# Performance work log

Measured on AMD Instinct MI355X. Metric: run time of the kernel, lower is better.

The kernel has to match this reference:

```python
import jax, jax.numpy as jnp
import numpy as np

EMB = 1024
H = 16
D = EMB // H  # 64
EPS = 1e-5
SM_SCALE = 1.0  # forward default sm_scale=1.0
CAUSAL = True
NEG = -1e30


def _layernorm(t, g, b):
    # LayerNorm over last dim (head_dim), per torch nn.LayerNorm(head_dim)
    m = jnp.mean(t, axis=-1, keepdims=True)
    v = jnp.mean(jnp.square(t - m), axis=-1, keepdims=True)
    return (t - m) * jax.lax.rsqrt(v + EPS) * g + b


def setup_inputs() -> dict:
    key = jax.random.key(0)
    ks = jax.random.split(key, 8)
    N, L = 2, 2048
    x = jax.random.normal(ks[0], (N, L, EMB), dtype=jnp.float32)
    mask = jnp.ones((N, L), dtype=jnp.int32)  # accepted but unused, as in the torch module
    s = 0.02
    Wq = jax.random.normal(ks[1], (EMB, EMB), dtype=jnp.float32) * s
    Wk = jax.random.normal(ks[2], (EMB, EMB), dtype=jnp.float32) * s
    Wv = jax.random.normal(ks[3], (EMB, EMB), dtype=jnp.float32) * s
    Wo = jax.random.normal(ks[4], (EMB, EMB), dtype=jnp.float32) * s
    bo = jnp.zeros((EMB,), dtype=jnp.float32)
    gq = jnp.ones((D,), dtype=jnp.float32)
    bq = jnp.zeros((D,), dtype=jnp.float32)
    gk = jnp.ones((D,), dtype=jnp.float32)
    bk = jnp.zeros((D,), dtype=jnp.float32)
    return {"x": x, "mask": mask, "Wq": Wq, "Wk": Wk, "Wv": Wv,
            "gq": gq, "bq": bq, "gk": gk, "bk": bk, "Wo": Wo, "bo": bo}


def reference(x, mask, Wq, Wk, Wv, gq, bq, gk, bk, Wo, bo):
    N, L, _ = x.shape
    # QKV projections (torch Linear: x @ W.T), split into heads -> [N, H, L, D]
    q = (x @ Wq.T).reshape(N, L, H, D).transpose(0, 2, 1, 3)
    k = (x @ Wk.T).reshape(N, L, H, D).transpose(0, 2, 1, 3)
    v = (x @ Wv.T).reshape(N, L, H, D).transpose(0, 2, 1, 3)
    # fused_q_norm variant: per-head LayerNorm on Q and K (fused into attention kernel)
    q = _layernorm(q, gq, bq)
    k = _layernorm(k, gk, bk)
    scores = jnp.einsum('nhld,nhmd->nhlm', q, k) * SM_SCALE  # [N,H,L,L]
    if CAUSAL:
        causal = jnp.tril(jnp.ones((L, L), dtype=bool))
        scores = jnp.where(causal, scores, NEG)
    attn = jax.nn.softmax(scores, axis=-1)
    out = jnp.einsum('nhlm,nhmd->nhld', attn, v)
    out = out.transpose(0, 2, 1, 3).reshape(N, L, EMB)
    return out @ Wo.T + bo
```

## Files before the change

kernel.cpp:

```cpp
#include <hip/hip_runtime.h>
#include <stdint.h>

typedef unsigned short u16;
typedef u16   u16x4    __attribute__((ext_vector_type(4)));
typedef u16   u16x8    __attribute__((ext_vector_type(8)));
typedef u16x8 u16x8_ma __attribute__((may_alias));
typedef __bf16 bf16x8  __attribute__((ext_vector_type(8)));
typedef float f32x4    __attribute__((ext_vector_type(4)));
typedef f32x4 f32x4_ma __attribute__((may_alias));

#define EMB    1024
#define NHEAD  16
#define HD     64
#define SEQ    2048
#define NBATCH 2
#define ROWS   (NBATCH*SEQ)
#define SATT   72

__device__ __forceinline__ u16 f2b(float f) {
  uint32_t u; __builtin_memcpy(&u, &f, 4);
  u = u + 0x7fffu + ((u >> 16) & 1u);
  return (u16)(u >> 16);
}
__device__ __forceinline__ u16x8 ld8(const u16* p) { return *(const u16x8_ma*)p; }
__device__ __forceinline__ void  st8(u16* p, u16x8 v) { *(u16x8_ma*)p = v; }
__device__ __forceinline__ bf16x8 asbf(u16x8 v) {
  union { u16x8 u; bf16x8 b; } c; c.u = v; return c.b;
}
__device__ __forceinline__ uint32_t cvtpk(float a, float b) {
  uint32_t r;
  asm("v_cvt_pk_bf16_f32 %0, %1, %2" : "=v"(r) : "v"(a), "v"(b));
  return r;
}
__device__ __forceinline__ void async_cp16(const u16* g, u16* l) {
  __builtin_amdgcn_global_load_lds(
      (const __attribute__((address_space(1))) void*)g,
      (__attribute__((address_space(3))) void*)l, 16, 0, 0);
}

__global__ __launch_bounds__(256) void cvt_all(
    const float* __restrict__ x,
    const float* __restrict__ w0, const float* __restrict__ w1,
    const float* __restrict__ w2, const float* __restrict__ w3,
    u16* __restrict__ xd, u16* __restrict__ d0, u16* __restrict__ d1,
    u16* __restrict__ d2, u16* __restrict__ d3)
{
  int bid = blockIdx.x;
  const float* s; u16* d; int off;
  if (bid < 4096) { s = x; d = xd; off = bid; }
  else {
    int t = bid - 4096; int m = t >> 10; off = t & 1023;
    switch (m) {
      case 0: s = w0; d = d0; break;
      case 1: s = w1; d = d1; break;
      case 2: s = w2; d = d2; break;
      default: s = w3; d = d3; break;
    }
  }
  size_t i = ((size_t)off * 256 + threadIdx.x) * 4;
  f32x4 v = *(const f32x4_ma*)(s + i);
  u16x4 o;
  #pragma unroll
  for (int j = 0; j < 4; j++) o[j] = f2b(v[j]);
  *(u16x4*)(d + i) = o;
}

template<int AMODE>
__device__ __forceinline__ void gemm_acc_128x128(
    const u16* __restrict__ A, const u16* __restrict__ B,
    int m0, int n0, u16* As, u16* Bs, f32x4 acc[4][4])
{
  const int tid  = threadIdx.x;
  const int lane = tid & 63;
  const int wave = tid >> 6;
  const int wm   = (wave >> 1) * 64;
  const int wn   = (wave & 1) * 64;
  const int ar   = tid >> 2;
  const int ac   = (tid & 3) * 8;
  const int lm   = lane & 15;
  const int lk   = (lane >> 4) * 8;

  #pragma unroll
  for (int i = 0; i < 4; i++)
    #pragma unroll
    for (int j = 0; j < 4; j++)
      #pragma unroll
      for (int e = 0; e < 4; e++) acc[i][j][e] = 0.f;

  for (int k0 = 0; k0 < EMB; k0 += 64) {
    size_t a0[2], a1[2];
    #pragma unroll
    for (int pnl = 0; pnl < 2; pnl++) {
      int kc = k0 + pnl * 32 + ac;
      if (AMODE == 0) {
        a0[pnl] = (size_t)(m0 + ar)      * EMB + kc;
        a1[pnl] = (size_t)(m0 + ar + 64) * EMB + kc;
      } else {
        int h = kc >> 6, d = kc & 63;
        int r0 = m0 + ar, r1 = m0 + ar + 64;
        a0[pnl] = (((size_t)((r0 >> 11) * NHEAD + h)) * SEQ + (r0 & (SEQ-1))) * HD + d;
        a1[pnl] = (((size_t)((r1 >> 11) * NHEAD + h)) * SEQ + (r1 & (SEQ-1))) * HD + d;
      }
    }
    __syncthreads();
    #pragma unroll
    for (int pnl = 0; pnl < 2; pnl++) {
      const int pb = pnl * 4096;
      async_cp16(A + a0[pnl], As + pb + tid * 8);
      async_cp16(A + a1[pnl], As + pb + (tid + 256) * 8);
      async_cp16(B + (size_t)(n0 + ar)      * EMB + k0 + pnl * 32 + ac, Bs + pb + tid * 8);
      async_cp16(B + (size_t)(n0 + ar + 64) * EMB + k0 + pnl * 32 + ac, Bs + pb + (tid + 256) * 8);
    }
    __syncthreads();

    #pragma unroll
    for (int pnl = 0; pnl < 2; pnl++) {
      const int pb = pnl * 4096;
      bf16x8 af[4], bfr[4];
      #pragma unroll
      for (int i = 0; i < 4; i++)
        af[i] = asbf(ld8(As + pb + (wm + i * 16 + lm) * 32 + lk));
      #pragma unroll
      for (int j = 0; j < 4; j++)
        bfr[j] = asbf(ld8(Bs + pb + (wn + j * 16 + lm) * 32 + lk));
      #pragma unroll
      for (int i = 0; i < 4; i++)
        #pragma unroll
        for (int j = 0; j < 4; j++)
          acc[i][j] = __builtin_amdgcn_mfma_f32_16x16x32_bf16(af[i], bfr[j], acc[i][j], 0, 0, 0);
    }
  }
}

__device__ __forceinline__ void epilogue_scatter_ln(
    f32x4 acc[4][4], u16* dst, int m0, int n0, int head_base, int Hdst,
    const float* g, const float* b, int do_ln)
{
  const int lane = threadIdx.x & 63, wave = threadIdx.x >> 6;
  const int wm = (wave >> 1) * 64, wn = (wave & 1) * 64;
  const int lm = lane & 15, quad = lane >> 4;

  float gv[4], bv[4];
  #pragma unroll
  for (int j = 0; j < 4; j++) { gv[j] = g[j * 16 + lm]; bv[j] = b[j * 16 + lm]; }

  #pragma unroll
  for (int i = 0; i < 4; i++)
    #pragma unroll
    for (int r = 0; r < 4; r++) {
      float val[4];
      #pragma unroll
      for (int j = 0; j < 4; j++) val[j] = acc[i][j][r];
      if (do_ln) {
        float s = val[0] + val[1] + val[2] + val[3];
        #pragma unroll
        for (int o = 8; o >= 1; o >>= 1) s += __shfl_xor(s, o, 64);
        float mean = s * (1.f / 64.f);
        float ss = 0.f;
        #pragma unroll
        for (int j = 0; j < 4; j++) { val[j] -= mean; ss += val[j] * val[j]; }
        #pragma unroll
        for (int o = 8; o >= 1; o >>= 1) ss += __shfl_xor(ss, o, 64);
        float inv = rsqrtf(ss * (1.f / 64.f) + 1e-5f);
        #pragma unroll
        for (int j = 0; j < 4; j++) val[j] = val[j] * inv * gv[j] + bv[j];
      }
      int row = m0 + wm + i * 16 + quad * 4 + r;
      int bn = row >> 11, l = row & (SEQ - 1);
      #pragma unroll
      for (int j = 0; j < 4; j++) {
        int col = n0 + wn + j * 16 + lm;
        int hl = (col >> 6) - head_base, d = col & 63;
        dst[(((size_t)(bn * Hdst + hl)) * SEQ + l) * HD + d] = f2b(val[j]);
      }
    }
}

__global__ __launch_bounds__(256) void gemm_qkv(
    const u16* __restrict__ x,
    const u16* __restrict__ Wq, const u16* __restrict__ Wk, const u16* __restrict__ Wv,
    const float* __restrict__ gq, const float* __restrict__ bq,
    const float* __restrict__ gk, const float* __restrict__ bk,
    u16* __restrict__ qd, u16* __restrict__ kb, u16* __restrict__ vb)
{
  __shared__ __align__(16) u16 As[128 * 64];
  __shared__ __align__(16) u16 Bs[128 * 64];
  const u16* W; u16* dst; const float* g; const float* b; int ln;
  if (blockIdx.z == 0)      { W = Wq; dst = qd; g = gq; b = bq; ln = 1; }
  else if (blockIdx.z == 1) { W = Wk; dst = kb; g = gk; b = bk; ln = 1; }
  else                      { W = Wv; dst = vb; g = gq; b = bq; ln = 0; }
  const int m0 = blockIdx.y * 128, n0 = blockIdx.x * 128;
  f32x4 acc[4][4];
  gemm_acc_128x128<0>(x, W, m0, n0, As, Bs, acc);
  epilogue_scatter_ln(acc, dst, m0, n0, 0, NHEAD, g, b, ln);
}

__global__ __launch_bounds__(256) void gemm_q(
    const u16* __restrict__ x, const u16* __restrict__ Wq,
    const float* __restrict__ gq, const float* __restrict__ bq,
    u16* __restrict__ qd)
{
  __shared__ __align__(16) u16 As[128 * 64];
  __shared__ __align__(16) u16 Bs[128 * 64];
  const int m0 = blockIdx.y * 128, n0 = blockIdx.x * 128;
  f32x4 acc[4][4];
  gemm_acc_128x128<0>(x, Wq, m0, n0, As, Bs, acc);
  epilogue_scatter_ln(acc, qd, m0, n0, 0, NHEAD, gq, bq, 1);
}
__global__ __launch_bounds__(256) void gemm_kv(
    const u16* __restrict__ x,
    const u16* __restrict__ Wk, const u16* __restrict__ Wv,
    const float* __restrict__ gk, const float* __restrict__ bk,
    u16* __restrict__ k, u16* __restrict__ v, int head_lo, int hpp)
{
  __shared__ __align__(16) u16 As[128 * 64];
  __shared__ __align__(16) u16 Bs[128 * 64];
  const int m0 = blockIdx.y * 128, n0 = blockIdx.x * 128;
  const u16* W = (blockIdx.z == 0 ? Wk : Wv) + (size_t)head_lo * HD * EMB;
  u16* dst = (blockIdx.z == 0) ? k : v;
  f32x4 acc[4][4];
  gemm_acc_128x128<0>(x, W, m0, n0, As, Bs, acc);
  epilogue_scatter_ln(acc, dst, m0, n0, 0, hpp, gk, bk, blockIdx.z == 0);
}

__global__ __launch_bounds__(256, 4) void attn(
    u16* qd, const u16* __restrict__ K, const u16* __restrict__ V,
    int head_lo, int hpp)
{
  __shared__ __align__(16) u16 Ks[2][64 * SATT];
  __shared__ __align__(16) u16 Vts[2][64 * 64];

  const int hl = blockIdx.y, n = blockIdx.z;
  const int perm = (7 * blockIdx.x + (hl & 7) + 8 * n) & 31;
  const int p = perm ^ (31 * (hl >> 3));
  const int tid = threadIdx.x, lane = tid & 63, wave = tid >> 6;
  const int lm = lane & 15, quad = lane >> 4, lk = quad * 8;
  u16* Qh = qd + ((size_t)(n * NHEAD + head_lo + hl)) * SEQ * HD;
  const u16* Kh = K + ((size_t)(n * hpp + hl)) * SEQ * HD;
  const u16* Vh = V + ((size_t)(n * hpp + hl)) * SEQ * HD;

  const int sr = tid >> 3;
  const int sc = (tid & 7) * 8;
  const int vswz = tid & 7;

  bf16x8 aq[2];
  #pragma unroll
  for (int ks = 0; ks < 2; ++ks)
    aq[ks] = asbf(ld8(Qh + (size_t)(p * 64 + wave * 16 + lm) * HD + ks * 32 + lk));

  u16x8 kr0, kr1, vr0, vr1;
  kr0 = ld8(Kh + (size_t)(sr)      * HD + sc);
  kr1 = ld8(Kh + (size_t)(sr + 32) * HD + sc);
  vr0 = ld8(Vh + (size_t)(sr)      * HD + sc);
  vr1 = ld8(Vh + (size_t)(sr + 32) * HD + sc);
  st8(&Ks[0][sr * SATT + sc], kr0);
  st8(&Ks[0][(sr + 32) * SATT + sc], kr1);
  #pragma unroll
  for (int jj = 0; jj < 8; jj++) {
    int d = sc + jj;
    Vts[0][d * 64 + (((sr >> 3) ^ vswz) * 8) + (sr & 7)]        = vr0[jj];
    Vts[0][d * 64 + ((((sr + 32) >> 3) ^ vswz) * 8) + (sr & 7)] = vr1[jj];
  }
  kr0 = ld8(Kh + (size_t)(64 + sr)      * HD + sc);
  kr1 = ld8(Kh + (size_t)(64 + sr + 32) * HD + sc);
  vr0 = ld8(Vh + (size_t)(64 + sr)      * HD + sc);
  vr1 = ld8(Vh + (size_t)(64 + sr + 32) * HD + sc);
  __syncthreads();

  f32x4 oacc[4];
  #pragma unroll
  for (int j = 0; j < 4; j++)
    #pragma unroll
    for (int e = 0; e < 4; e++) oacc[j][e] = 0.f;
  float m_i = -1e30f, psum = 0.f;

  const int idx0 = (((quad & 1) * 2) * 16 + lm) * 4;
  const int idx1 = idx0 + 64;
  const int qrow = p * 64 + wave * 16 + lm;

  for (int t = 0; t <= p; ++t) {
    const int cur = t & 1;
    if (t < p) {
      const int nb = 1 - cur;
      st8(&Ks[nb][sr * SATT + sc], kr0);
      st8(&Ks[nb][(sr + 32) * SATT + sc], kr1);
      #pragma unroll
      for (int jj = 0; jj < 8; jj++) {
        int d = sc + jj;
        Vts[nb][d * 64 + (((sr >> 3) ^ vswz) * 8) + (sr & 7)]        = vr0[jj];
        Vts[nb][d * 64 + ((((sr + 32) >> 3) ^ vswz) * 8) + (sr & 7)] = vr1[jj];
      }
      if (t + 1 < p) {
        const size_t base = (size_t)(t + 2) * 64;
        kr0 = ld8(Kh + (base + sr)      * HD + sc);
        kr1 = ld8(Kh + (base + sr + 32) * HD + sc);
        vr0 = ld8(Vh + (base + sr)      * HD + sc);
        vr1 = ld8(Vh + (base + sr + 32) * HD + sc);
      }
    }

    f32x4 s[4];
    #pragma unroll
    for (int j = 0; j < 4; j++)
      #pragma unroll
      for (int e = 0; e < 4; e++) s[j][e] = 0.f;
    __builtin_amdgcn_s_setprio(1);
    #pragma unroll
    for (int ks = 0; ks < 2; ++ks)
      #pragma unroll
      for (int j = 0; j < 4; j++) {
        bf16x8 ak = asbf(ld8(&Ks[cur][(j * 16 + lm) * SATT + ks * 32 + lk]));
        s[j] = __builtin_amdgcn_mfma_f32_16x16x32_bf16(ak, aq[ks], s[j], 0, 0, 0);
      }
    __builtin_amdgcn_s_setprio(0);

    if (t == p) {
      #pragma unroll
      for (int j = 0; j < 4; j++)
        #pragma unroll
        for (int r = 0; r < 4; r++)
          if (t * 64 + j * 16 + quad * 4 + r > qrow) s[j][r] = -1e30f;
    }

    float mx = fmaxf(fmaxf(s[0][0], s[0][1]), fmaxf(s[0][2], s[0][3]));
    #pragma unroll
    for (int j = 1; j < 4; j++)
      mx = fmaxf(mx, fmaxf(fmaxf(s[j][0], s[j][1]), fmaxf(s[j][2], s[j][3])));
    mx = fmaxf(mx, __shfl_xor(mx, 16, 64));
    mx = fmaxf(mx, __shfl_xor(mx, 32, 64));
    const float mnew = fmaxf(m_i, mx);
    const float alpha = __expf(m_i - mnew);
    m_i = mnew;
    float part = 0.f;
    #pragma unroll
    for (int j = 0; j < 4; j++)
      #pragma unroll
      for (int r = 0; r < 4; r++) {
        float pv = __expf(s[j][r] - mnew);
        s[j][r] = pv;
        part += pv;
      }
    psum = psum * alpha + part;

    float ar_[4];
    #pragma unroll
    for (int r = 0; r < 4; r++)
      ar_[r] = __shfl(alpha, (lane & 48) | (quad * 4 + r), 64);
    #pragma unroll
    for (int j = 0; j < 4; j++)
      #pragma unroll
      for (int r = 0; r < 4; r++) oacc[j][r] *= ar_[r];

    uint32_t u[8];
    #pragma unroll
    for (int j = 0; j < 4; j++) {
      u[2 * j]     = cvtpk(s[j][0], s[j][1]);
      u[2 * j + 1] = cvtpk(s[j][2], s[j][3]);
    }

    __builtin_amdgcn_s_setprio(1);
    #pragma unroll
    for (int ks = 0; ks < 2; ++ks) {
      union { uint32_t w[4]; bf16x8 v; } cv;
      #pragma unroll
      for (int w = 0; w < 4; w++) {
        int lo = __builtin_amdgcn_ds_bpermute(w < 2 ? idx0 : idx1,
                                              (int)u[ks * 4 + (w & 1)]);
        int hi = __builtin_amdgcn_ds_bpermute(w < 2 ? idx0 : idx1,
                                              (int)u[ks * 4 + 2 + (w & 1)]);
        cv.w[w] = (quad < 2) ? (uint32_t)lo : (uint32_t)hi;
      }
      bf16x8 ap = cv.v;
      #pragma unroll
      for (int j = 0; j < 4; j++) {
        int dg = 2 * j + (lm >> 3);
        int g  = (ks * 4 + quad) ^ (dg & 7);
        bf16x8 bv = asbf(ld8(&Vts[cur][(j * 16 + lm) * 64 + g * 8]));
        oacc[j] = __builtin_amdgcn_mfma_f32_16x16x32_bf16(ap, bv, oacc[j], 0, 0, 0);
      }
    }
    __builtin_amdgcn_s_setprio(0);
    __syncthreads();
  }

  float s_ = psum;
  s_ += __shfl_xor(s_, 16, 64);
  s_ += __shfl_xor(s_, 32, 64);
  const float inv = 1.0f / s_;
  float ir_[4];
  #pragma unroll
  for (int r = 0; r < 4; r++)
    ir_[r] = __shfl(inv, (lane & 48) | (quad * 4 + r), 64);
  #pragma unroll
  for (int r = 0; r < 4; r++) {
    const int row = p * 64 + wave * 16 + quad * 4 + r;
    #pragma unroll
    for (int j = 0; j < 4; j++)
      Qh[(size_t)row * HD + j * 16 + lm] = f2b(oacc[j][r] * ir_[r]);
  }
}

__global__ __launch_bounds__(256) void gemm_out(
    const u16* __restrict__ ao, const u16* __restrict__ Wo,
    const float* __restrict__ bo, float* __restrict__ out)
{
  __shared__ __align__(16) u16 As[64 * 64];
  __shared__ __align__(16) u16 Bs[128 * 64];
  const int m0 = blockIdx.y * 64, n0 = blockIdx.x * 128;
  const int tid  = threadIdx.x;
  const int lane = tid & 63;
  const int wave = tid >> 6;
  const int wm   = (wave >> 1) * 32;
  const int wn   = (wave & 1) * 64;
  const int ar   = tid >> 2;
  const int ac   = (tid & 3) * 8;
  const int lm   = lane & 15;
  const int lk   = (lane >> 4) * 8;

  f32x4 acc[2][4];
  #pragma unroll
  for (int i = 0; i < 2; i++)
    #pragma unroll
    for (int j = 0; j < 4; j++)
      #pragma unroll
      for (int e = 0; e < 4; e++) acc[i][j][e] = 0.f;

  for (int k0 = 0; k0 < EMB; k0 += 64) {
    size_t aoff[2];
    #pragma unroll
    for (int pnl = 0; pnl < 2; pnl++) {
      int kc = k0 + pnl * 32 + ac, h = kc >> 6, d = kc & 63;
      int r0 = m0 + ar;
      aoff[pnl] = (((size_t)((r0 >> 11) * NHEAD + h)) * SEQ + (r0 & (SEQ-1))) * HD + d;
    }
    __syncthreads();
    #pragma unroll
    for (int pnl = 0; pnl < 2; pnl++) {
      async_cp16(ao + aoff[pnl], As + pnl * 2048 + tid * 8);
      async_cp16(Wo + (size_t)(n0 + ar)      * EMB + k0 + pnl * 32 + ac, Bs + pnl * 4096 + tid * 8);
      async_cp16(Wo + (size_t)(n0 + ar + 64) * EMB + k0 + pnl * 32 + ac, Bs + pnl * 4096 + (tid + 256) * 8);
    }
    __syncthreads();

    #pragma unroll
    for (int pnl = 0; pnl < 2; pnl++) {
      bf16x8 af[2], bfr[4];
      #pragma unroll
      for (int i = 0; i < 2; i++)
        af[i] = asbf(ld8(As + pnl * 2048 + (wm + i * 16 + lm) * 32 + lk));
      #pragma unroll
      for (int j = 0; j < 4; j++)
        bfr[j] = asbf(ld8(Bs + pnl * 4096 + (wn + j * 16 + lm) * 32 + lk));
      #pragma unroll
      for (int i = 0; i < 2; i++)
        #pragma unroll
        for (int j = 0; j < 4; j++)
          acc[i][j] = __builtin_amdgcn_mfma_f32_16x16x32_bf16(af[i], bfr[j], acc[i][j], 0, 0, 0);
    }
  }

  const int quad = lane >> 4;
  #pragma unroll
  for (int j = 0; j < 4; j++) {
    int col = n0 + wn + j * 16 + lm;
    float bias = bo[col];
    #pragma unroll
    for (int i = 0; i < 2; i++)
      #pragma unroll
      for (int r = 0; r < 4; r++) {
        int row = m0 + wm + i * 16 + quad * 4 + r;
        out[(size_t)row * EMB + col] = acc[i][j][r] + bias;
      }
  }
}

extern "C" void kernel_launch(void* const* d_in, const int* in_sizes, int n_in,
                              void* d_out, int out_size, void* d_ws, size_t ws_size,
                              hipStream_t stream)
{
  const float* xf  = (const float*)d_in[0];
  const float* Wqf = (const float*)d_in[2];
  const float* Wkf = (const float*)d_in[3];
  const float* Wvf = (const float*)d_in[4];
  const float* gq  = (const float*)d_in[5];
  const float* bq  = (const float*)d_in[6];
  const float* gk  = (const float*)d_in[7];
  const float* bk  = (const float*)d_in[8];
  const float* Wof = (const float*)d_in[9];
  const float* bo  = (const float*)d_in[10];

  const size_t MB = 1u << 20;
  u16* xb  = (u16*)d_ws;
  u16* wqb = xb  + (size_t)ROWS * EMB;
  u16* wkb = wqb + (size_t)EMB * EMB;
  u16* wvb = wkb + (size_t)EMB * EMB;
  u16* wob = wvb + (size_t)EMB * EMB;
  u16* kvbase = wob + (size_t)EMB * EMB;

  size_t avail = (ws_size > 16 * MB) ? ws_size - 16 * MB : 2 * MB;
  int hpp = NHEAD;
  while ((size_t)hpp * MB > avail && hpp > 2) hpp >>= 1;
  const size_t kv_elems = (size_t)hpp * NBATCH * SEQ * HD;
  u16* kbuf = kvbase;
  u16* vbuf = kbuf + kv_elems;

  u16* qd = (u16*)d_in[0];
  float* out = (float*)d_out;

  cvt_all<<<dim3(8192), 256, 0, stream>>>(xf, Wqf, Wkf, Wvf, Wof,
                                          xb, wqb, wkb, wvb, wob);
  if (hpp == NHEAD) {
    gemm_qkv<<<dim3(8, 32, 3), 256, 0, stream>>>(xb, wqb, wkb, wvb,
                                                 gq, bq, gk, bk,
                                                 qd, kbuf, vbuf);
    attn<<<dim3(32, NHEAD, NBATCH), 256, 0, stream>>>(qd, kbuf, vbuf, 0, NHEAD);
  } else {
    gemm_q<<<dim3(8, 32), 256, 0, stream>>>(xb, wqb, gq, bq, qd);
    for (int g = 0; g < NHEAD / hpp; ++g) {
      gemm_kv<<<dim3(hpp / 2, 32, 2), 256, 0, stream>>>(xb, wkb, wvb, gk, bk,
                                                        kbuf, vbuf, g * hpp, hpp);
      attn<<<dim3(32, hpp, NBATCH), 256, 0, stream>>>(qd, kbuf, vbuf, g * hpp, hpp);
    }
  }
  gemm_out<<<dim3(8, 64), 256, 0, stream>>>(qd, wob, bo, out);
}
```

Measured before the change: 217.5 us.

## Store V transposed from projection epilogue to avoid in-kernel LDS transpose

```diff
diff --git a/kernel.cpp b/kernel.cpp
--- a/kernel.cpp
+++ b/kernel.cpp
@@ -134,7 +134,7 @@
 
 __device__ __forceinline__ void epilogue_scatter_ln(
     f32x4 acc[4][4], u16* dst, int m0, int n0, int head_base, int Hdst,
-    const float* g, const float* b, int do_ln)
+    const float* g, const float* b, int do_ln, int vt)
 {
   const int lane = threadIdx.x & 63, wave = threadIdx.x >> 6;
   const int wm = (wave >> 1) * 64, wn = (wave & 1) * 64;
@@ -171,7 +171,10 @@
       for (int j = 0; j < 4; j++) {
         int col = n0 + wn + j * 16 + lm;
         int hl = (col >> 6) - head_base, d = col & 63;
-        dst[(((size_t)(bn * Hdst + hl)) * SEQ + l) * HD + d] = f2b(val[j]);
+        if (vt)
+          dst[(((size_t)(bn * Hdst + hl)) * HD + d) * SEQ + l] = f2b(val[j]);
+        else
+          dst[(((size_t)(bn * Hdst + hl)) * SEQ + l) * HD + d] = f2b(val[j]);
       }
     }
 }
@@ -185,14 +188,14 @@
 {
   __shared__ __align__(16) u16 As[128 * 64];
   __shared__ __align__(16) u16 Bs[128 * 64];
-  const u16* W; u16* dst; const float* g; const float* b; int ln;
-  if (blockIdx.z == 0)      { W = Wq; dst = qd; g = gq; b = bq; ln = 1; }
-  else if (blockIdx.z == 1) { W = Wk; dst = kb; g = gk; b = bk; ln = 1; }
-  else                      { W = Wv; dst = vb; g = gq; b = bq; ln = 0; }
+  const u16* W; u16* dst; const float* g; const float* b; int ln, vt;
+  if (blockIdx.z == 0)      { W = Wq; dst = qd; g = gq; b = bq; ln = 1; vt = 0; }
+  else if (blockIdx.z == 1) { W = Wk; dst = kb; g = gk; b = bk; ln = 1; vt = 0; }
+  else                      { W = Wv; dst = vb; g = gq; b = bq; ln = 0; vt = 1; }
   const int m0 = blockIdx.y * 128, n0 = blockIdx.x * 128;
   f32x4 acc[4][4];
   gemm_acc_128x128<0>(x, W, m0, n0, As, Bs, acc);
-  epilogue_scatter_ln(acc, dst, m0, n0, 0, NHEAD, g, b, ln);
+  epilogue_scatter_ln(acc, dst, m0, n0, 0, NHEAD, g, b, ln, vt);
 }
 
 __global__ __launch_bounds__(256) void gemm_q(
@@ -205,7 +208,7 @@
   const int m0 = blockIdx.y * 128, n0 = blockIdx.x * 128;
   f32x4 acc[4][4];
   gemm_acc_128x128<0>(x, Wq, m0, n0, As, Bs, acc);
-  epilogue_scatter_ln(acc, qd, m0, n0, 0, NHEAD, gq, bq, 1);
+  epilogue_scatter_ln(acc, qd, m0, n0, 0, NHEAD, gq, bq, 1, 0);
 }
 __global__ __launch_bounds__(256) void gemm_kv(
     const u16* __restrict__ x,
@@ -220,7 +223,8 @@
   u16* dst = (blockIdx.z == 0) ? k : v;
   f32x4 acc[4][4];
   gemm_acc_128x128<0>(x, W, m0, n0, As, Bs, acc);
-  epilogue_scatter_ln(acc, dst, m0, n0, 0, hpp, gk, bk, blockIdx.z == 0);
+  epilogue_scatter_ln(acc, dst, m0, n0, 0, hpp, gk, bk, blockIdx.z == 0,
+                      blockIdx.z == 1);
 }
 
 __global__ __launch_bounds__(256, 4) void attn(
@@ -228,7 +232,7 @@
     int head_lo, int hpp)
 {
   __shared__ __align__(16) u16 Ks[2][64 * SATT];
-  __shared__ __align__(16) u16 Vts[2][64 * 64];
+  __shared__ __align__(16) u16 Vt[2][64 * SATT];
 
   const int hl = blockIdx.y, n = blockIdx.z;
   const int perm = (7 * blockIdx.x + (hl & 7) + 8 * n) & 31;
@@ -237,11 +241,12 @@
   const int lm = lane & 15, quad = lane >> 4, lk = quad * 8;
   u16* Qh = qd + ((size_t)(n * NHEAD + head_lo + hl)) * SEQ * HD;
   const u16* Kh = K + ((size_t)(n * hpp + hl)) * SEQ * HD;
-  const u16* Vh = V + ((size_t)(n * hpp + hl)) * SEQ * HD;
+  const u16* Vh = V + ((size_t)(n * hpp + hl)) * HD * SEQ;
 
   const int sr = tid >> 3;
   const int sc = (tid & 7) * 8;
-  const int vswz = tid & 7;
+  const int vd = tid >> 2;
+  const int vc = (tid & 3) * 16;
 
   bf16x8 aq[2];
   #pragma unroll
@@ -251,20 +256,16 @@
   u16x8 kr0, kr1, vr0, vr1;
   kr0 = ld8(Kh + (size_t)(sr)      * HD + sc);
   kr1 = ld8(Kh + (size_t)(sr + 32) * HD + sc);
-  vr0 = ld8(Vh + (size_t)(sr)      * HD + sc);
-  vr1 = ld8(Vh + (size_t)(sr + 32) * HD + sc);
+  vr0 = ld8(Vh + (size_t)vd * SEQ + vc);
+  vr1 = ld8(Vh + (size_t)vd * SEQ + vc + 8);
   st8(&Ks[0][sr * SATT + sc], kr0);
   st8(&Ks[0][(sr + 32) * SATT + sc], kr1);
-  #pragma unroll
-  for (int jj = 0; jj < 8; jj++) {
-    int d = sc + jj;
-    Vts[0][d * 64 + (((sr >> 3) ^ vswz) * 8) + (sr & 7)]        = vr0[jj];
-    Vts[0][d * 64 + ((((sr + 32) >> 3) ^ vswz) * 8) + (sr & 7)] = vr1[jj];
-  }
+  st8(&Vt[0][vd * SATT + vc], vr0);
+  st8(&Vt[0][vd * SATT + vc + 8], vr1);
   kr0 = ld8(Kh + (size_t)(64 + sr)      * HD + sc);
   kr1 = ld8(Kh + (size_t)(64 + sr + 32) * HD + sc);
-  vr0 = ld8(Vh + (size_t)(64 + sr)      * HD + sc);
-  vr1 = ld8(Vh + (size_t)(64 + sr + 32) * HD + sc);
+  vr0 = ld8(Vh + (size_t)vd * SEQ + 64 + vc);
+  vr1 = ld8(Vh + (size_t)vd * SEQ + 64 + vc + 8);
   __syncthreads();
 
   f32x4 oacc[4];
@@ -284,18 +285,14 @@
       const int nb = 1 - cur;
       st8(&Ks[nb][sr * SATT + sc], kr0);
       st8(&Ks[nb][(sr + 32) * SATT + sc], kr1);
-      #pragma unroll
-      for (int jj = 0; jj < 8; jj++) {
-        int d = sc + jj;
-        Vts[nb][d * 64 + (((sr >> 3) ^ vswz) * 8) + (sr & 7)]        = vr0[jj];
-        Vts[nb][d * 64 + ((((sr + 32) >> 3) ^ vswz) * 8) + (sr & 7)] = vr1[jj];
-      }
+      st8(&Vt[nb][vd * SATT + vc], vr0);
+      st8(&Vt[nb][vd * SATT + vc + 8], vr1);
       if (t + 1 < p) {
         const size_t base = (size_t)(t + 2) * 64;
         kr0 = ld8(Kh + (base + sr)      * HD + sc);
         kr1 = ld8(Kh + (base + sr + 32) * HD + sc);
-        vr0 = ld8(Vh + (base + sr)      * HD + sc);
-        vr1 = ld8(Vh + (base + sr + 32) * HD + sc);
+        vr0 = ld8(Vh + (size_t)vd * SEQ + base + vc);
+        vr1 = ld8(Vh + (size_t)vd * SEQ + base + vc + 8);
       }
     }
 
@@ -373,9 +370,7 @@
       bf16x8 ap = cv.v;
       #pragma unroll
       for (int j = 0; j < 4; j++) {
-        int dg = 2 * j + (lm >> 3);
-        int g  = (ks * 4 + quad) ^ (dg & 7);
-        bf16x8 bv = asbf(ld8(&Vts[cur][(j * 16 + lm) * 64 + g * 8]));
+        bf16x8 bv = asbf(ld8(&Vt[cur][(j * 16 + lm) * SATT + ks * 32 + lk]));
         oacc[j] = __builtin_amdgcn_mfma_f32_16x16x32_bf16(ap, bv, oacc[j], 0, 0, 0);
       }
     }
```

Result: no change. 221.1 us (+1.6%).
